# Performance work log

Measured on AMD Instinct MI355X. Metric: run time of the kernel, lower is better.

## Reference

```python
import jax, jax.numpy as jnp
import numpy as np

B, S, D = 4, 2048, 512
H = 8
HD = D // H  # 64


def setup_inputs() -> dict:
    key = jax.random.key(0)
    ks = jax.random.split(key, 11)
    scale = 1.0 / np.sqrt(D)
    inp = {
        "query": jax.random.normal(ks[0], (B, S, D), dtype=jnp.float32),
        "key": jax.random.normal(ks[1], (B, S, D), dtype=jnp.float32),
        "value": jax.random.normal(ks[2], (B, S, D), dtype=jnp.float32),
        "Wq": jax.random.normal(ks[3], (D, D), dtype=jnp.float32) * scale,
        "bq": jnp.zeros((D,), dtype=jnp.float32),
        "Wk": jax.random.normal(ks[4], (D, D), dtype=jnp.float32) * scale,
        "bk": jnp.zeros((D,), dtype=jnp.float32),
        "Wv": jax.random.normal(ks[5], (D, D), dtype=jnp.float32) * scale,
        "bv": jnp.zeros((D,), dtype=jnp.float32),
        "Wo": jax.random.normal(ks[6], (D, D), dtype=jnp.float32) * scale,
        "bo": jnp.zeros((D,), dtype=jnp.float32),
    }
    return inp


def reference(query, key, value, Wq, bq, Wk, bk, Wv, bv, Wo, bo):
    # Linear projections (torch Linear: x @ W.T + b)
    q = (query @ Wq.T + bq).reshape(B, -1, H, HD).transpose(0, 2, 1, 3)  # [B,H,Sq,HD]
    k = (key   @ Wk.T + bk).reshape(B, -1, H, HD).transpose(0, 2, 1, 3)  # [B,H,Sk,HD]
    v = (value @ Wv.T + bv).reshape(B, -1, H, HD).transpose(0, 2, 1, 3)  # [B,H,Sk,HD]

    # Chunked loop in original is mathematically identical to full attention
    scores = jnp.einsum('bhqd,bhkd->bhqk', q, k) / np.sqrt(HD)  # [B,H,Sq,Sk]
    attn = jax.nn.softmax(scores, axis=-1)
    out = jnp.einsum('bhqk,bhkd->bhqd', attn, v)  # [B,H,Sq,HD]
    out = out.transpose(0, 2, 1, 3).reshape(B, -1, D)  # [B,Sq,D]
    return out @ Wo.T + bo
```

## Files before the change

kernel.cpp:

```cpp
#include <hip/hip_runtime.h>
#include <hip/hip_bf16.h>

typedef __attribute__((ext_vector_type(8))) short bf16x8;
typedef __attribute__((ext_vector_type(4))) float f32x4;
typedef __attribute__((ext_vector_type(16))) float f32x16;
typedef __attribute__((ext_vector_type(4))) unsigned int u32x4;

#define MFMA16(a, b, c) __builtin_amdgcn_mfma_f32_16x16x32_bf16((a), (b), (c), 0, 0, 0)
#define MFMA32(a, b, c) __builtin_amdgcn_mfma_f32_32x32x16_bf16((a), (b), (c), 0, 0, 0)

static constexpr int BATCH = 4, S = 2048, DMODEL = 512, H = 8, HD = 64;
static constexpr int M = BATCH * S;

__device__ __forceinline__ float fmax3(float a, float b, float c) {
  return fmaxf(fmaxf(a, b), c);
}

__device__ __forceinline__ float rexp2(float x) {
  float r;
  asm("v_exp_f32 %0, %1" : "=v"(r) : "v"(x));
  return r;
}

__device__ __forceinline__ short f2b(float f) {
  unsigned int u = __builtin_bit_cast(unsigned int, f);
  unsigned int r = (u + 0x7fffu + ((u >> 16) & 1u)) >> 16;
  return (short)r;
}

__device__ __forceinline__ bf16x8 cvt8(const float4& a, const float4& b) {
  bf16x8 r;
  r[0] = f2b(a.x); r[1] = f2b(a.y); r[2] = f2b(a.z); r[3] = f2b(a.w);
  r[4] = f2b(b.x); r[5] = f2b(b.y); r[6] = f2b(b.z); r[7] = f2b(b.w);
  return r;
}

__device__ __forceinline__ void glds16(const void* g, void* l) {
  __builtin_amdgcn_global_load_lds(
      (const __attribute__((address_space(1))) unsigned int*)g,
      (__attribute__((address_space(3))) unsigned int*)l, 16, 0, 0);
}

__global__ __launch_bounds__(256) void convert_w(
    const float* __restrict__ Wq, const float* __restrict__ Wk,
    const float* __restrict__ Wv, const float* __restrict__ Wo,
    short* __restrict__ Wb) {
  const float* src = (blockIdx.y == 0) ? Wq : (blockIdx.y == 1) ? Wk
                   : (blockIdx.y == 2) ? Wv : Wo;
  short* dst = Wb + blockIdx.y * (DMODEL * DMODEL);
  int i = (blockIdx.x * 256 + threadIdx.x) * 8;
  float4 a = *(const float4*)&src[i];
  float4 b = *(const float4*)&src[i + 4];
  *(bf16x8*)&dst[i] = cvt8(a, b);
}

__global__ __launch_bounds__(256) void proj_gemm(
    const float* __restrict__ Aq, const float* __restrict__ Ak, const float* __restrict__ Av,
    const short* __restrict__ Wb,
    const float* __restrict__ bq, const float* __restrict__ bk, const float* __restrict__ bv,
    short* __restrict__ Qp, short* __restrict__ Kp, short* __restrict__ Vp) {
  const int which = blockIdx.y;
  const float* A    = (which == 0) ? Aq : (which == 1) ? Ak : Av;
  const short* W    = Wb + which * (DMODEL * DMODEL);
  const float* bias = (which == 0) ? bq : (which == 1) ? bk : bv;
  short* dst        = (which == 0) ? Qp : (which == 1) ? Kp : Vp;

  const int tm = blockIdx.x & 63;
  const int tn = blockIdx.x >> 6;
  const int m0 = tm * 128, n0 = tn * 128;
  const int t = threadIdx.x;
  const int lane = t & 63, w = t >> 6;
  const int g = lane >> 4, c = lane & 15;
  const int wr = w >> 1, wc = w & 1;

  __shared__ __align__(16) short As[2][128 * 32];
  __shared__ __align__(16) short Bs[2][128 * 32];

  f32x4 acc[4][4];
  const f32x4 fz = {0.f, 0.f, 0.f, 0.f};
#pragma unroll
  for (int i = 0; i < 4; ++i)
#pragma unroll
    for (int j = 0; j < 4; ++j) acc[i][j] = fz;

  const int r0 = t >> 2, c0 = (t & 3) * 8;
  const int r1 = r0 + 64;

  const short* Bsrc0 = W + (n0 + w * 16 + (lane >> 2)) * DMODEL + (lane & 3) * 8;
  const short* Bsrc1 = Bsrc0 + 64 * DMODEL;

  {
    glds16(Bsrc0, &Bs[0][w * 512]);
    glds16(Bsrc1, &Bs[0][2048 + w * 512]);
    float4 a0 = *(const float4*)&A[(m0 + r0) * DMODEL + c0];
    float4 a1 = *(const float4*)&A[(m0 + r0) * DMODEL + c0 + 4];
    float4 a2 = *(const float4*)&A[(m0 + r1) * DMODEL + c0];
    float4 a3 = *(const float4*)&A[(m0 + r1) * DMODEL + c0 + 4];
    *(bf16x8*)&As[0][r0 * 32 + c0] = cvt8(a0, a1);
    *(bf16x8*)&As[0][r1 * 32 + c0] = cvt8(a2, a3);
    __syncthreads();
  }

  for (int kt = 0; kt < 16; ++kt) {
    const int cur = kt & 1, nxt = cur ^ 1;
    float4 a0, a1, a2, a3;
    const bool pf = (kt < 15);
    if (pf) {
      const int k0 = (kt + 1) * 32;
      glds16(Bsrc0 + k0, &Bs[nxt][w * 512]);
      glds16(Bsrc1 + k0, &Bs[nxt][2048 + w * 512]);
      a0 = *(const float4*)&A[(m0 + r0) * DMODEL + k0 + c0];
      a1 = *(const float4*)&A[(m0 + r0) * DMODEL + k0 + c0 + 4];
      a2 = *(const float4*)&A[(m0 + r1) * DMODEL + k0 + c0];
      a3 = *(const float4*)&A[(m0 + r1) * DMODEL + k0 + c0 + 4];
    }

    bf16x8 af[4], bfr[4];
#pragma unroll
    for (int i = 0; i < 4; ++i)
      af[i] = *(const bf16x8*)&As[cur][(wr * 64 + i * 16 + c) * 32 + g * 8];
#pragma unroll
    for (int j = 0; j < 4; ++j)
      bfr[j] = *(const bf16x8*)&Bs[cur][(wc * 64 + j * 16 + c) * 32 + g * 8];
    if (which == 2) {
#pragma unroll
      for (int i = 0; i < 4; ++i)
#pragma unroll
        for (int j = 0; j < 4; ++j)
          acc[i][j] = MFMA16(bfr[j], af[i], acc[i][j]);
    } else {
#pragma unroll
      for (int i = 0; i < 4; ++i)
#pragma unroll
        for (int j = 0; j < 4; ++j)
          acc[i][j] = MFMA16(af[i], bfr[j], acc[i][j]);
    }

    if (pf) {
      *(bf16x8*)&As[nxt][r0 * 32 + c0] = cvt8(a0, a1);
      *(bf16x8*)&As[nxt][r1 * 32 + c0] = cvt8(a2, a3);
    }
    __syncthreads();
  }

  if (which == 2) {
#pragma unroll
    for (int j = 0; j < 4; ++j) {
#pragma unroll
      for (int r = 0; r < 4; ++r) {
        const int n = n0 + wc * 64 + j * 16 + g * 4 + r;
        const int h = n >> 6, hd = n & 63;
        const float bn = bias[n];
#pragma unroll
        for (int i = 0; i < 4; ++i) {
          const int m = m0 + wr * 64 + i * 16 + c;
          const int bb = m >> 11, s = m & (S - 1);
          dst[((bb * H + h) * HD + hd) * S + s] = f2b(acc[i][j][r] + bn);
        }
      }
    }
  } else {
#pragma unroll
    for (int i = 0; i < 4; ++i) {
#pragma unroll
      for (int j = 0; j < 4; ++j) {
        const int n = n0 + wc * 64 + j * 16 + c;
        const int h = n >> 6, hd = n & 63;
        const float bn = bias[n];
#pragma unroll
        for (int r = 0; r < 4; ++r) {
          const int m = m0 + wr * 64 + i * 16 + g * 4 + r;
          const int bb = m >> 11, s = m & (S - 1);
          dst[((bb * H + h) * S + s) * HD + hd] = f2b(acc[i][j][r] + bn);
        }
      }
    }
  }
}

__global__ __launch_bounds__(256) void out_gemm(
    const short* __restrict__ Am, const short* __restrict__ W,
    const float* __restrict__ bias, float* __restrict__ Out) {
  const int tm = blockIdx.x & 63;
  const int tn = blockIdx.x >> 6;
  const int m0 = tm * 128, n0 = tn * 128;
  const int t = threadIdx.x;
  const int lane = t & 63, w = t >> 6;
  const int g = lane >> 4, c = lane & 15;
  const int wr = w >> 1, wc = w & 1;

  __shared__ __align__(16) short As[2][128 * 32];
  __shared__ __align__(16) short Bs[2][128 * 32];

  f32x4 acc[4][4];
  const f32x4 fz = {0.f, 0.f, 0.f, 0.f};
#pragma unroll
  for (int i = 0; i < 4; ++i)
#pragma unroll
    for (int j = 0; j < 4; ++j) acc[i][j] = fz;

  const short* Asrc0 = Am + (m0 + w * 16 + (lane >> 2)) * DMODEL + (lane & 3) * 8;
  const short* Asrc1 = Asrc0 + 64 * DMODEL;
  const short* Bsrc0 = W + (n0 + w * 16 + (lane >> 2)) * DMODEL + (lane & 3) * 8;
  const short* Bsrc1 = Bsrc0 + 64 * DMODEL;

  glds16(Asrc0, &As[0][w * 512]);
  glds16(Asrc1, &As[0][2048 + w * 512]);
  glds16(Bsrc0, &Bs[0][w * 512]);
  glds16(Bsrc1, &Bs[0][2048 + w * 512]);
  __syncthreads();

  for (int kt = 0; kt < 16; ++kt) {
    const int cur = kt & 1, nxt = cur ^ 1;
    if (kt < 15) {
      const int k0 = (kt + 1) * 32;
      glds16(Asrc0 + k0, &As[nxt][w * 512]);
      glds16(Asrc1 + k0, &As[nxt][2048 + w * 512]);
      glds16(Bsrc0 + k0, &Bs[nxt][w * 512]);
      glds16(Bsrc1 + k0, &Bs[nxt][2048 + w * 512]);
    }

    bf16x8 af[4], bfr[4];
#pragma unroll
    for (int i = 0; i < 4; ++i)
      af[i] = *(const bf16x8*)&As[cur][(wr * 64 + i * 16 + c) * 32 + g * 8];
#pragma unroll
    for (int j = 0; j < 4; ++j)
      bfr[j] = *(const bf16x8*)&Bs[cur][(wc * 64 + j * 16 + c) * 32 + g * 8];
#pragma unroll
    for (int i = 0; i < 4; ++i)
#pragma unroll
      for (int j = 0; j < 4; ++j)
        acc[i][j] = MFMA16(af[i], bfr[j], acc[i][j]);

    __syncthreads();
  }

#pragma unroll
  for (int i = 0; i < 4; ++i) {
#pragma unroll
    for (int j = 0; j < 4; ++j) {
      const int n = n0 + wc * 64 + j * 16 + c;
      const float bn = bias[n];
#pragma unroll
      for (int r = 0; r < 4; ++r) {
        const int m = m0 + wr * 64 + i * 16 + g * 4 + r;
        Out[m * DMODEL + n] = acc[i][j][r] + bn;
      }
    }
  }
}

__global__ __launch_bounds__(256, 2) void attn_kernel(
    const short* __restrict__ Qp, const short* __restrict__ Kp,
    const short* __restrict__ VTp, short* __restrict__ att) {
  const int bid = blockIdx.x;
  const int swzb = (bid & 7) * 64 + (bid >> 3);
  const int qt = swzb & 15;
  const int bh = swzb >> 4;
  const int b = bh >> 3, h = bh & 7;
  const short* Q  = Qp  + bh * (S * HD);
  const char*  Kg = (const char*)(Kp  + bh * (S * HD));
  const char*  Vg = (const char*)(VTp + bh * (HD * S));

  const int t = threadIdx.x;
  const int lane = t & 63, w = t >> 6;
  const int l31 = lane & 31, hi = lane >> 5;
  const int q0 = qt * 128 + w * 32;

  __shared__ __align__(16) char smem[2 * 16384];

  const int rowi = lane >> 3;
  const int swzs = ((lane & 7) * 16) ^ (rowi << 4);
  const char* ksrc0 = Kg + (w * 16 + rowi) * 128 + swzs;
  const char* ksrc1 = ksrc0 + 8 * 128;
  const char* vsrc0 = Vg + (w * 16 + rowi) * 4096 + swzs;
  const char* vsrc1 = vsrc0 + 8 * 4096;

  bf16x8 qf[4];
#pragma unroll
  for (int ks = 0; ks < 4; ++ks)
    qf[ks] = *(const bf16x8*)&Q[(q0 + l31) * HD + ks * 16 + hi * 8];

  bf16x8 ones;
#pragma unroll
  for (int i = 0; i < 8; ++i) ones[i] = (short)0x3F80;

  f32x16 o0, o1, osum, fz16;
#pragma unroll
  for (int i = 0; i < 16; ++i) { o0[i] = 0.f; o1[i] = 0.f; osum[i] = 0.f; fz16[i] = 0.f; }
  float mst = -1e30f;

  glds16(ksrc0, smem + w * 2048);
  glds16(ksrc1, smem + w * 2048 + 1024);
  glds16(vsrc0, smem + 8192 + w * 2048);
  glds16(vsrc1, smem + 8192 + w * 2048 + 1024);
  __syncthreads();

  const float SCL = 0.18033688011112042f;
  const int fswz = (l31 & 7) << 4;

#pragma unroll 2
  for (int kt = 0; kt < 32; ++kt) {
    const int cb = (kt & 1) * 16384;

    if (kt < 31) {
      char* nb = smem + (cb ^ 16384);
      const size_t ko = (size_t)(kt + 1) * 8192;
      const size_t vo = (size_t)(kt + 1) * 128;
      glds16(ksrc0 + ko, nb + w * 2048);
      glds16(ksrc1 + ko, nb + w * 2048 + 1024);
      glds16(vsrc0 + vo, nb + 8192 + w * 2048);
      glds16(vsrc1 + vo, nb + 8192 + w * 2048 + 1024);
    }

    f32x16 sa0, sa1;
    __builtin_amdgcn_s_setprio(1);
    {
      const int col0 = (hi * 16) ^ fswz;
      const bf16x8 k00 = *(const bf16x8*)&smem[cb + l31 * 128 + col0];
      const bf16x8 k10 = *(const bf16x8*)&smem[cb + (32 + l31) * 128 + col0];
      sa0 = MFMA32(k00, qf[0], fz16);
      sa1 = MFMA32(k10, qf[0], fz16);
    }
#pragma unroll
    for (int ks = 1; ks < 4; ++ks) {
      const int col = (ks * 32 + hi * 16) ^ fswz;
      const bf16x8 k0 = *(const bf16x8*)&smem[cb + l31 * 128 + col];
      const bf16x8 k1 = *(const bf16x8*)&smem[cb + (32 + l31) * 128 + col];
      sa0 = MFMA32(k0, qf[ks], sa0);
      sa1 = MFMA32(k1, qf[ks], sa1);
    }
    __builtin_amdgcn_s_setprio(0);

    float u0 = fmax3(fmax3(sa0[0], sa0[1], sa0[2]), fmax3(sa0[3], sa0[4], sa0[5]),
                     fmax3(sa0[6], sa0[7], sa0[8]));
    float u1 = fmax3(fmax3(sa0[9], sa0[10], sa0[11]), fmax3(sa0[12], sa0[13], sa0[14]),
                     sa0[15]);
    float u2 = fmax3(fmax3(sa1[0], sa1[1], sa1[2]), fmax3(sa1[3], sa1[4], sa1[5]),
                     fmax3(sa1[6], sa1[7], sa1[8]));
    float u3 = fmax3(fmax3(sa1[9], sa1[10], sa1[11]), fmax3(sa1[12], sa1[13], sa1[14]),
                     sa1[15]);
    float mloc = fmax3(fmaxf(u0, u1), u2, u3);
    const float mx = fmaxf(mloc, __shfl_xor(mloc, 32, 64));
    const float mxs = mx * SCL;

    if (!__all(mxs - mst <= 8.0f)) {
      const float mn = fmaxf(mst, mxs);
      const float corr = rexp2(mst - mn);
      osum[0] *= corr;
#pragma unroll
      for (int i = 0; i < 16; ++i) { o0[i] *= corr; o1[i] *= corr; }
      mst = mn;
    }

#pragma unroll
    for (int i = 0; i < 16; ++i) {
      sa0[i] = rexp2(__builtin_fmaf(sa0[i], SCL, -mst));
      sa1[i] = rexp2(__builtin_fmaf(sa1[i], SCL, -mst));
    }

    unsigned int wrd0[8], wrd1[8];
#pragma unroll
    for (int i = 0; i < 8; ++i) {
      asm("v_cvt_pk_bf16_f32 %0, %1, %2" : "=v"(wrd0[i]) : "v"(sa0[2 * i]), "v"(sa0[2 * i + 1]));
      asm("v_cvt_pk_bf16_f32 %0, %1, %2" : "=v"(wrd1[i]) : "v"(sa1[2 * i]), "v"(sa1[2 * i + 1]));
    }

    __builtin_amdgcn_s_setprio(1);
#pragma unroll
    for (int ks = 0; ks < 4; ++ks) {
      const int i0 = (ks & 1) * 4;
      unsigned int a0 = (ks < 2) ? wrd0[i0 + 0] : wrd1[i0 + 0];
      unsigned int b0 = (ks < 2) ? wrd0[i0 + 2] : wrd1[i0 + 2];
      unsigned int a1 = (ks < 2) ? wrd0[i0 + 1] : wrd1[i0 + 1];
      unsigned int b1 = (ks < 2) ? wrd0[i0 + 3] : wrd1[i0 + 3];
      asm("v_permlane32_swap_b32 %0, %1" : "+v"(a0), "+v"(b0));
      asm("v_permlane32_swap_b32 %0, %1" : "+v"(a1), "+v"(b1));
      u32x4 fw;
      fw[0] = a0; fw[1] = a1; fw[2] = b0; fw[3] = b1;
      const bf16x8 pfrag = __builtin_bit_cast(bf16x8, fw);
      const int col = (ks * 32 + hi * 16) ^ fswz;
      const bf16x8 va0 = *(const bf16x8*)&smem[cb + 8192 + l31 * 128 + col];
      const bf16x8 va1 = *(const bf16x8*)&smem[cb + 8192 + (32 + l31) * 128 + col];
      o0 = MFMA32(va0, pfrag, o0);
      o1 = MFMA32(va1, pfrag, o1);
      osum = MFMA32(ones, pfrag, osum);
    }
    __builtin_amdgcn_s_setprio(0);

    __syncthreads();
  }

  const float inv = 1.0f / osum[0];
  short* arow = att + (b * S + q0 + l31) * DMODEL + h * HD;
#pragma unroll
  for (int dt = 0; dt < 2; ++dt) {
#pragma unroll
    for (int rr = 0; rr < 4; ++rr) {
      float v0 = (dt ? o1[4 * rr + 0] : o0[4 * rr + 0]) * inv;
      float v1 = (dt ? o1[4 * rr + 1] : o0[4 * rr + 1]) * inv;
      float v2 = (dt ? o1[4 * rr + 2] : o0[4 * rr + 2]) * inv;
      float v3 = (dt ? o1[4 * rr + 3] : o0[4 * rr + 3]) * inv;
      unsigned int w0, w1;
      asm("v_cvt_pk_bf16_f32 %0, %1, %2" : "=v"(w0) : "v"(v0), "v"(v1));
      asm("v_cvt_pk_bf16_f32 %0, %1, %2" : "=v"(w1) : "v"(v2), "v"(v3));
      uint2 pk2;
      pk2.x = w0; pk2.y = w1;
      *(uint2*)&arow[dt * 32 + rr * 8 + hi * 4] = pk2;
    }
  }
}

extern "C" void kernel_launch(void* const* d_in, const int* in_sizes, int n_in,
                              void* d_out, int out_size, void* d_ws, size_t ws_size,
                              hipStream_t stream) {
  const float* query = (const float*)d_in[0];
  const float* key_  = (const float*)d_in[1];
  const float* value = (const float*)d_in[2];
  const float* Wq = (const float*)d_in[3];
  const float* bq = (const float*)d_in[4];
  const float* Wk = (const float*)d_in[5];
  const float* bk = (const float*)d_in[6];
  const float* Wv = (const float*)d_in[7];
  const float* bv = (const float*)d_in[8];
  const float* Wo = (const float*)d_in[9];
  const float* bo = (const float*)d_in[10];
  float* out = (float*)d_out;

  char* ws = (char*)d_ws;
  const size_t WB_BYTES  = (size_t)4 * DMODEL * DMODEL * 2;
  const size_t MAT_BYTES = (size_t)M * DMODEL * 2;
  short* Wb  = (short*)ws;
  short* Qp  = (short*)(ws + WB_BYTES);
  short* Kp  = (short*)(ws + WB_BYTES + MAT_BYTES);
  short* Vp  = (short*)(ws + WB_BYTES + 2 * MAT_BYTES);
  short* att = (short*)(ws + WB_BYTES + 3 * MAT_BYTES);

  convert_w<<<dim3(128, 4), 256, 0, stream>>>(Wq, Wk, Wv, Wo, Wb);
  proj_gemm<<<dim3(256, 3), 256, 0, stream>>>(query, key_, value, Wb, bq, bk, bv, Qp, Kp, Vp);
  attn_kernel<<<dim3(512), 256, 0, stream>>>(Qp, Kp, Vp, att);
  out_gemm<<<dim3(256), 256, 0, stream>>>(att, Wb + 3 * DMODEL * DMODEL, bo, out);
}
```

Measured before the change: 111.1 us.

## Triple-buffer global-to-LDS loads with explicit vmcnt waits in all kernels

Converts the double-buffered LDS pipelines in the QKV projection, output GEMM and attention kernels to three-stage rotating buffers that prefetch two tiles ahead. The full __syncthreads at each iteration end becomes a partial s_waitcnt vmcnt plus a raw s_barrier at the iteration start, with sched_barriers to keep the compiler from reordering. The aim is to hide global load latency and remove one barrier per iteration. The cost is more LDS per block, which may lower occupancy in the attention kernel (48KB with 2 blocks per CU targeted). Correctness relies on the hand-set vmcnt counts matching the number of outstanding loads.

```diff
diff --git a/kernel.cpp b/kernel.cpp
--- a/kernel.cpp
+++ b/kernel.cpp
@@ -11,6 +11,10 @@
 
 static constexpr int BATCH = 4, S = 2048, DMODEL = 512, H = 8, HD = 64;
 static constexpr int M = BATCH * S;
+
+#define WAIT_VM(N) asm volatile("s_waitcnt vmcnt(" #N ")" ::: "memory")
+#define WAIT_VM_LGKM(N) asm volatile("s_waitcnt vmcnt(" #N ") lgkmcnt(0)" ::: "memory")
+#define SCHEDB() __builtin_amdgcn_sched_barrier(0)
 
 __device__ __forceinline__ float fmax3(float a, float b, float c) {
   return fmaxf(fmaxf(a, b), c);
@@ -74,7 +78,7 @@
   const int wr = w >> 1, wc = w & 1;
 
   __shared__ __align__(16) short As[2][128 * 32];
-  __shared__ __align__(16) short Bs[2][128 * 32];
+  __shared__ __align__(16) short Bs[3][128 * 32];
 
   f32x4 acc[4][4];
   const f32x4 fz = {0.f, 0.f, 0.f, 0.f};
@@ -90,38 +94,46 @@
   const short* Bsrc1 = Bsrc0 + 64 * DMODEL;
 
   {
-    glds16(Bsrc0, &Bs[0][w * 512]);
-    glds16(Bsrc1, &Bs[0][2048 + w * 512]);
     float4 a0 = *(const float4*)&A[(m0 + r0) * DMODEL + c0];
     float4 a1 = *(const float4*)&A[(m0 + r0) * DMODEL + c0 + 4];
     float4 a2 = *(const float4*)&A[(m0 + r1) * DMODEL + c0];
     float4 a3 = *(const float4*)&A[(m0 + r1) * DMODEL + c0 + 4];
+    glds16(Bsrc0, &Bs[0][w * 512]);
+    glds16(Bsrc1, &Bs[0][2048 + w * 512]);
+    glds16(Bsrc0 + 32, &Bs[1][w * 512]);
+    glds16(Bsrc1 + 32, &Bs[1][2048 + w * 512]);
     *(bf16x8*)&As[0][r0 * 32 + c0] = cvt8(a0, a1);
     *(bf16x8*)&As[0][r1 * 32 + c0] = cvt8(a2, a3);
-    __syncthreads();
-  }
-
+  }
+
+  int ob0 = 0, ob1 = 1, ob2 = 2;
   for (int kt = 0; kt < 16; ++kt) {
-    const int cur = kt & 1, nxt = cur ^ 1;
+    if (kt == 15) { WAIT_VM_LGKM(0); } else { WAIT_VM_LGKM(2); }
+    __builtin_amdgcn_s_barrier();
+    SCHEDB();
+
     float4 a0, a1, a2, a3;
-    const bool pf = (kt < 15);
-    if (pf) {
+    if (kt < 15) {
       const int k0 = (kt + 1) * 32;
-      glds16(Bsrc0 + k0, &Bs[nxt][w * 512]);
-      glds16(Bsrc1 + k0, &Bs[nxt][2048 + w * 512]);
       a0 = *(const float4*)&A[(m0 + r0) * DMODEL + k0 + c0];
       a1 = *(const float4*)&A[(m0 + r0) * DMODEL + k0 + c0 + 4];
       a2 = *(const float4*)&A[(m0 + r1) * DMODEL + k0 + c0];
       a3 = *(const float4*)&A[(m0 + r1) * DMODEL + k0 + c0 + 4];
     }
+    if (kt < 14) {
+      const int k0 = (kt + 2) * 32;
+      glds16(Bsrc0 + k0, &Bs[ob2][w * 512]);
+      glds16(Bsrc1 + k0, &Bs[ob2][2048 + w * 512]);
+    }
+    SCHEDB();
 
     bf16x8 af[4], bfr[4];
 #pragma unroll
     for (int i = 0; i < 4; ++i)
-      af[i] = *(const bf16x8*)&As[cur][(wr * 64 + i * 16 + c) * 32 + g * 8];
+      af[i] = *(const bf16x8*)&As[kt & 1][(wr * 64 + i * 16 + c) * 32 + g * 8];
 #pragma unroll
     for (int j = 0; j < 4; ++j)
-      bfr[j] = *(const bf16x8*)&Bs[cur][(wc * 64 + j * 16 + c) * 32 + g * 8];
+      bfr[j] = *(const bf16x8*)&Bs[ob0][(wc * 64 + j * 16 + c) * 32 + g * 8];
     if (which == 2) {
 #pragma unroll
       for (int i = 0; i < 4; ++i)
@@ -136,11 +148,11 @@
           acc[i][j] = MFMA16(af[i], bfr[j], acc[i][j]);
     }
 
-    if (pf) {
-      *(bf16x8*)&As[nxt][r0 * 32 + c0] = cvt8(a0, a1);
-      *(bf16x8*)&As[nxt][r1 * 32 + c0] = cvt8(a2, a3);
-    }
-    __syncthreads();
+    if (kt < 15) {
+      *(bf16x8*)&As[(kt + 1) & 1][r0 * 32 + c0] = cvt8(a0, a1);
+      *(bf16x8*)&As[(kt + 1) & 1][r1 * 32 + c0] = cvt8(a2, a3);
+    }
+    const int tmp = ob0; ob0 = ob1; ob1 = ob2; ob2 = tmp;
   }
 
   if (which == 2) {
@@ -189,8 +201,7 @@
   const int g = lane >> 4, c = lane & 15;
   const int wr = w >> 1, wc = w & 1;
 
-  __shared__ __align__(16) short As[2][128 * 32];
-  __shared__ __align__(16) short Bs[2][128 * 32];
+  __shared__ __align__(16) short SM[3][2 * 128 * 32];
 
   f32x4 acc[4][4];
   const f32x4 fz = {0.f, 0.f, 0.f, 0.f};
@@ -204,36 +215,42 @@
   const short* Bsrc0 = W + (n0 + w * 16 + (lane >> 2)) * DMODEL + (lane & 3) * 8;
   const short* Bsrc1 = Bsrc0 + 64 * DMODEL;
 
-  glds16(Asrc0, &As[0][w * 512]);
-  glds16(Asrc1, &As[0][2048 + w * 512]);
-  glds16(Bsrc0, &Bs[0][w * 512]);
-  glds16(Bsrc1, &Bs[0][2048 + w * 512]);
-  __syncthreads();
-
+#pragma unroll
+  for (int tt = 0; tt < 2; ++tt) {
+    glds16(Asrc0 + tt * 32, &SM[tt][w * 512]);
+    glds16(Asrc1 + tt * 32, &SM[tt][2048 + w * 512]);
+    glds16(Bsrc0 + tt * 32, &SM[tt][4096 + w * 512]);
+    glds16(Bsrc1 + tt * 32, &SM[tt][4096 + 2048 + w * 512]);
+  }
+
+  int ob0 = 0, ob1 = 1, ob2 = 2;
   for (int kt = 0; kt < 16; ++kt) {
-    const int cur = kt & 1, nxt = cur ^ 1;
-    if (kt < 15) {
-      const int k0 = (kt + 1) * 32;
-      glds16(Asrc0 + k0, &As[nxt][w * 512]);
-      glds16(Asrc1 + k0, &As[nxt][2048 + w * 512]);
-      glds16(Bsrc0 + k0, &Bs[nxt][w * 512]);
-      glds16(Bsrc1 + k0, &Bs[nxt][2048 + w * 512]);
-    }
+    if (kt == 15) { WAIT_VM(0); } else { WAIT_VM(4); }
+    __builtin_amdgcn_s_barrier();
+    SCHEDB();
+    if (kt < 14) {
+      const int k0 = (kt + 2) * 32;
+      glds16(Asrc0 + k0, &SM[ob2][w * 512]);
+      glds16(Asrc1 + k0, &SM[ob2][2048 + w * 512]);
+      glds16(Bsrc0 + k0, &SM[ob2][4096 + w * 512]);
+      glds16(Bsrc1 + k0, &SM[ob2][4096 + 2048 + w * 512]);
+    }
+    SCHEDB();
 
     bf16x8 af[4], bfr[4];
 #pragma unroll
     for (int i = 0; i < 4; ++i)
-      af[i] = *(const bf16x8*)&As[cur][(wr * 64 + i * 16 + c) * 32 + g * 8];
+      af[i] = *(const bf16x8*)&SM[ob0][(wr * 64 + i * 16 + c) * 32 + g * 8];
 #pragma unroll
     for (int j = 0; j < 4; ++j)
-      bfr[j] = *(const bf16x8*)&Bs[cur][(wc * 64 + j * 16 + c) * 32 + g * 8];
+      bfr[j] = *(const bf16x8*)&SM[ob0][4096 + (wc * 64 + j * 16 + c) * 32 + g * 8];
 #pragma unroll
     for (int i = 0; i < 4; ++i)
 #pragma unroll
       for (int j = 0; j < 4; ++j)
         acc[i][j] = MFMA16(af[i], bfr[j], acc[i][j]);
 
-    __syncthreads();
+    const int tmp = ob0; ob0 = ob1; ob1 = ob2; ob2 = tmp;
   }
 
 #pragma unroll
@@ -268,7 +285,7 @@
   const int l31 = lane & 31, hi = lane >> 5;
   const int q0 = qt * 128 + w * 32;
 
-  __shared__ __align__(16) char smem[2 * 16384];
+  __shared__ __align__(16) char smem[3 * 16384];
 
   const int rowi = lane >> 3;
   const int swzs = ((lane & 7) * 16) ^ (rowi << 4);
@@ -291,29 +308,36 @@
   for (int i = 0; i < 16; ++i) { o0[i] = 0.f; o1[i] = 0.f; osum[i] = 0.f; fz16[i] = 0.f; }
   float mst = -1e30f;
 
-  glds16(ksrc0, smem + w * 2048);
-  glds16(ksrc1, smem + w * 2048 + 1024);
-  glds16(vsrc0, smem + 8192 + w * 2048);
-  glds16(vsrc1, smem + 8192 + w * 2048 + 1024);
-  __syncthreads();
+#pragma unroll
+  for (int tt = 0; tt < 2; ++tt) {
+    char* nb = smem + tt * 16384;
+    glds16(ksrc0 + (size_t)tt * 8192, nb + w * 2048);
+    glds16(ksrc1 + (size_t)tt * 8192, nb + w * 2048 + 1024);
+    glds16(vsrc0 + (size_t)tt * 128, nb + 8192 + w * 2048);
+    glds16(vsrc1 + (size_t)tt * 128, nb + 8192 + w * 2048 + 1024);
+  }
 
   const float SCL = 0.18033688011112042f;
   const int fswz = (l31 & 7) << 4;
 
+  int ob0 = 0, ob1 = 16384, ob2 = 32768;
 #pragma unroll 2
   for (int kt = 0; kt < 32; ++kt) {
-    const int cb = (kt & 1) * 16384;
-
-    if (kt < 31) {
-      char* nb = smem + (cb ^ 16384);
-      const size_t ko = (size_t)(kt + 1) * 8192;
-      const size_t vo = (size_t)(kt + 1) * 128;
+    if (kt == 31) { WAIT_VM(0); } else { WAIT_VM(4); }
+    __builtin_amdgcn_s_barrier();
+    SCHEDB();
+    if (kt < 30) {
+      char* nb = smem + ob2;
+      const size_t ko = (size_t)(kt + 2) * 8192;
+      const size_t vo = (size_t)(kt + 2) * 128;
       glds16(ksrc0 + ko, nb + w * 2048);
       glds16(ksrc1 + ko, nb + w * 2048 + 1024);
       glds16(vsrc0 + vo, nb + 8192 + w * 2048);
       glds16(vsrc1 + vo, nb + 8192 + w * 2048 + 1024);
     }
-
+    SCHEDB();
+
+    const int cb = ob0;
     f32x16 sa0, sa1;
     __builtin_amdgcn_s_setprio(1);
     {
@@ -389,7 +413,7 @@
     }
     __builtin_amdgcn_s_setprio(0);
 
-    __syncthreads();
+    const int tmp = ob0; ob0 = ob1; ob1 = ob2; ob2 = tmp;
   }
 
   const float inv = 1.0f / osum[0];
```

Result: faster. 105.9 us (-4.7%).
